# Kernel tuning notes

Measured on AMD Instinct MI355X. Metric: run time of the kernel, lower is better.

Reference implementation:

```python
import jax, jax.numpy as jnp
import numpy as np

DIM = 256
FEATURE_SCALE = 4
NMS_THRESHOLD = 8.0
PRE_NMS_TOPK = 2048
MAX_OUTPUT = 256
MIN_SCORE = 0.2


def conv3d_same(x, w, b):
    # x: [D,H,W,Cin], w: [3,3,3,Cin,Cout] -> [D,H,W,Cout], SAME padding (flax default)
    y = jax.lax.conv_general_dilated(
        x[None], w, window_strides=(1, 1, 1), padding="SAME",
        dimension_numbers=("NDHWC", "DHWIO", "NDHWC"))
    return y[0] + b


def setup_inputs() -> dict:
    key = jax.random.key(0)
    ks = jax.random.split(key, 8)
    D, H, W, C = 16, 64, 64, 256
    feature = jax.random.normal(ks[0], (D, H, W, C), jnp.float32)
    mask = jax.random.bernoulli(ks[1], 0.8, (D * FEATURE_SCALE, H * FEATURE_SCALE, W * FEATURE_SCALE))
    s3a = 1.0 / np.sqrt(27 * C)
    s3b = 1.0 / np.sqrt(27 * DIM)
    s1 = 1.0 / np.sqrt(DIM)
    w0 = jax.random.normal(ks[2], (3, 3, 3, C, DIM), jnp.float32) * s3a
    b0 = jnp.zeros((DIM,), jnp.float32)
    w1 = jax.random.normal(ks[3], (3, 3, 3, DIM, DIM), jnp.float32) * s3b
    b1 = jnp.zeros((DIM,), jnp.float32)
    w_logit = jax.random.normal(ks[4], (DIM, 1), jnp.float32) * s1
    b_logit = jnp.zeros((1,), jnp.float32)
    w_reg = jax.random.normal(ks[5], (DIM, 3), jnp.float32) * s1
    b_reg = jnp.zeros((3,), jnp.float32)
    return dict(feature=feature, mask=mask, w0=w0, b0=b0, w1=w1, b1=b1,
                w_logit=w_logit, b_logit=b_logit, w_reg=w_reg, b_reg=b_reg)


def reference(feature, mask, w0, b0, w1, b1, w_logit, b_logit, w_reg, b_reg):
    # ---- feature mixing: n_layers=2 of conv3d + gelu (flax gelu is approximate/tanh) ----
    x = jax.nn.gelu(conv3d_same(feature, w0, b0))
    x = jax.nn.gelu(conv3d_same(x, w1, b1))
    D, H, W = x.shape[:3]

    # ---- detection block: 1x1 convs are pointwise dense layers ----
    logits = (x @ w_logit + b_logit)[..., 0].reshape(-1)          # [N]
    regressions = (x @ w_reg + b_reg)                              # [D,H,W,3]
    ref_locs = (jnp.moveaxis(jnp.mgrid[:D, :H, :W], 0, -1) + 0.5) * FEATURE_SCALE
    pred_locs = (ref_locs + regressions * FEATURE_SCALE).reshape(-1, 3)  # [N,3]

    # ---- generate_predictions: sigmoid scores, pre-NMS top-k, greedy distance NMS ----
    scores = jax.nn.sigmoid(logits)
    top_scores, idx = jax.lax.top_k(scores, PRE_NMS_TOPK)          # sorted desc
    top_locs = pred_locs[idx]                                      # [K,3]
    d2 = ((top_locs[:, None, :] - top_locs[None, :, :]) ** 2).sum(-1)  # [K,K]
    th2 = NMS_THRESHOLD * NMS_THRESHOLD

    def step(suppressed, i):
        keep_i = (~suppressed[i]) & (top_scores[i] >= MIN_SCORE)
        suppressed = suppressed | (keep_i & (d2[i] < th2))
        return suppressed, keep_i

    _, keep = jax.lax.scan(step, jnp.zeros((PRE_NMS_TOPK,), bool), jnp.arange(PRE_NMS_TOPK))
    sel_scores = jnp.where(keep, top_scores, 0.0)
    out_scores, oidx = jax.lax.top_k(sel_scores, MAX_OUTPUT)       # [M]
    out_locs = top_locs[oidx]                                      # [M,3]

    # ---- mask gather: floor/clip/index, zero out-of-mask scores ----
    pli = jnp.floor(out_locs).astype(jnp.int32)
    bound = jnp.array(mask.shape, jnp.int32) - 1
    plc = jnp.clip(pli, 0, bound)
    in_range = (pli == plc).all(axis=1)
    masked = jnp.where(in_range, mask[plc[:, 0], plc[:, 1], plc[:, 2]], False)
    out_scores = jnp.where(masked, out_scores, 0.0)

    return jnp.concatenate([out_locs, out_scores[:, None]], axis=-1)  # [M,4] = (z,y,x,score)
```

## Files before the change

### kernel.cpp

```cpp
#include <hip/hip_runtime.h>
#include <math.h>

#define Dz 16
#define Hy 64
#define Wx 64
#define CHN 256
#define NVOX (Dz*Hy*Wx)
#define TOPK 2048
#define MAXOUT 256
#define CAND_CAP 4096
#define NBCAP 16

typedef __attribute__((ext_vector_type(8))) _Float16 h8;
typedef __attribute__((ext_vector_type(8))) unsigned short u16x8;
typedef __attribute__((ext_vector_type(4))) float f32x4;

__device__ __forceinline__ float gelu_tanh(float x) {
    return 0.5f*x*(1.0f + tanhf(0.7978845608028654f*(x + 0.044715f*x*x*x)));
}
__device__ __forceinline__ unsigned f2sort(float f) {
    unsigned u = __float_as_uint(f);
    return (u & 0x80000000u) ? ~u : (u | 0x80000000u);
}
__device__ __forceinline__ float sort2f(unsigned s) {
    unsigned u = (s & 0x80000000u) ? (s & 0x7fffffffu) : ~s;
    return __uint_as_float(u);
}

#define MFMA(d, a, b) d = __builtin_amdgcn_mfma_f32_16x16x32_f16(a, b, d, 0, 0, 0)

__global__ __launch_bounds__(256) void pack_w_kernel(const float* __restrict__ w0,
        const float* __restrict__ w1, u16x8* __restrict__ wpk0,
        u16x8* __restrict__ wpk1) {
    int id = blockIdx.x*256 + threadIdx.x;
    int l = (id >= 221184) ? 1 : 0;
    int r = id - l*221184;
    int lane = r & 63, ng = (r >> 6) & 15, kbg = (r >> 10) & 7, t = r >> 13;
    const float* w = l ? w1 : w0;
    u16x8* dst = l ? wpk1 : wpk0;
    h8 hv = {0,0,0,0,0,0,0,0}, lv = {0,0,0,0,0,0,0,0};
    #pragma unroll
    for (int j = 0; j < 8; ++j) {
        int k = kbg*32 + (lane >> 4)*8 + j;
        int co = ng*16 + (lane & 15);
        float v = w[((size_t)t*CHN + k)*CHN + co];
        _Float16 h = (_Float16)v;
        hv[j] = h;
        lv[j] = (_Float16)(v - (float)h);
    }
    size_t base = (((size_t)(t*8 + kbg)*16 + ng)*2)*64 + lane;
    dst[base]      = __builtin_bit_cast(u16x8, hv);
    dst[base + 64] = __builtin_bit_cast(u16x8, lv);
}

template<int LAYER>
__global__ __launch_bounds__(512, 4) void conv_kernel(
        const float* __restrict__ fsrc,
        const unsigned short* __restrict__ hhi, const unsigned short* __restrict__ hlo,
        const u16x8* __restrict__ wpk, const float* __restrict__ bias,
        unsigned short* __restrict__ ohi, unsigned short* __restrict__ olo,
        const float* __restrict__ wlog, const float* __restrict__ blog,
        const float* __restrict__ wreg, const float* __restrict__ breg,
        float* __restrict__ locs, unsigned long long* __restrict__ keys,
        unsigned* __restrict__ hist) {
    __shared__ h8 sm[4224];
    const int tid = threadIdx.x;
    const int lane = tid & 63, w = tid >> 6;
    const int yo = w >> 2, wn = w & 3;
    const int lr = lane & 15, lg = lane >> 4;
    const int z = blockIdx.y, y0 = blockIdx.x*2;

    f32x4 acc[4][4];
    #pragma unroll
    for (int m = 0; m < 4; ++m)
        #pragma unroll
        for (int n = 0; n < 4; ++n) acc[m][n] = (f32x4){0.f,0.f,0.f,0.f};

    for (int dz = 0; dz < 3; ++dz) {
        const int zz = z + dz - 1;
        for (int kc = 0; kc < 4; ++kc) {
            __syncthreads();
            if (LAYER == 0) {
                for (int cidx = tid; cidx < 2112; cidx += 512) {
                    int cd = cidx & 7;
                    int rr = cidx >> 3;
                    int r = rr % 66, iy = rr / 66;
                    int ygl = y0 - 1 + iy, xin = r - 1;
                    h8 hv = {0,0,0,0,0,0,0,0}, lv = {0,0,0,0,0,0,0,0};
                    if (((unsigned)zz < (unsigned)Dz) & ((unsigned)ygl < (unsigned)Hy)
                        & ((unsigned)xin < (unsigned)Wx)) {
                        const float* s = fsrc + ((size_t)((zz*Hy + ygl)*Wx + xin))*CHN
                                              + kc*64 + cd*8;
                        float4 t0 = *(const float4*)s;
                        float4 t1 = *(const float4*)(s + 4);
                        float vv[8] = {t0.x,t0.y,t0.z,t0.w,t1.x,t1.y,t1.z,t1.w};
                        #pragma unroll
                        for (int j = 0; j < 8; ++j) {
                            _Float16 h = (_Float16)vv[j];
                            hv[j] = h;
                            lv[j] = (_Float16)(vv[j] - (float)h);
                        }
                    }
                    int sl = cd ^ (r & 7);
                    sm[(iy*66 + r)*8 + sl] = hv;
                    sm[2112 + (iy*66 + r)*8 + sl] = lv;
                }
            } else {
                for (int cidx = tid; cidx < 4224; cidx += 512) {
                    int c = cidx & 7;
                    int rr = cidx >> 3;
                    int r = rr % 66, tt = rr / 66;
                    int p = tt >> 2, iy = tt & 3;
                    int ygl = y0 - 1 + iy, xin = r - 1;
                    u16x8 v = {0,0,0,0,0,0,0,0};
                    if (((unsigned)zz < (unsigned)Dz) & ((unsigned)ygl < (unsigned)Hy)
                        & ((unsigned)xin < (unsigned)Wx)) {
                        const unsigned short* bp = p ? hlo : hhi;
                        v = *(const u16x8*)(bp + ((size_t)((zz*Hy + ygl)*Wx + xin))*CHN
                                               + kc*64 + (size_t)((c ^ (r & 7)))*8);
                    }
                    sm[cidx] = __builtin_bit_cast(h8, v);
                }
            }
            __syncthreads();
            for (int dy = 0; dy < 3; ++dy) {
                const int iyA = yo + dy;
                const h8* As = sm + iyA*528;
                #pragma unroll
                for (int dx = 0; dx < 3; ++dx) {
                    const int tap = (dz*3 + dy)*3 + dx;
                    #pragma unroll
                    for (int kb = 0; kb < 2; ++kb) {
                        const int kbg = kc*2 + kb;
                        const u16x8* wb = wpk + ((size_t)(tap*8 + kbg)*32 + wn*8)*64 + lane;
                        h8 bh[4];
                        #pragma unroll
                        for (int n = 0; n < 4; ++n)
                            bh[n] = __builtin_bit_cast(h8, wb[(size_t)n*128]);
                        #pragma unroll
                        for (int m = 0; m < 4; ++m) {
                            const int r = m*16 + lr + dx;
                            const int sl = (kb*4 + lg) ^ (r & 7);
                            h8 ah = As[r*8 + sl];
                            h8 al = As[2112 + r*8 + sl];
                            #pragma unroll
                            for (int n = 0; n < 4; ++n) {
                                MFMA(acc[m][n], ah, bh[n]);
                                MFMA(acc[m][n], al, bh[n]);
                            }
                        }
                        h8 bl[4];
                        #pragma unroll
                        for (int n = 0; n < 4; ++n)
                            bl[n] = __builtin_bit_cast(h8, wb[(size_t)n*128 + 64]);
                        #pragma unroll
                        for (int m = 0; m < 4; ++m) {
                            const int r = m*16 + lr + dx;
                            const int sl = (kb*4 + lg) ^ (r & 7);
                            h8 ah = As[r*8 + sl];
                            #pragma unroll
                            for (int n = 0; n < 4; ++n) MFMA(acc[m][n], ah, bl[n]);
                        }
                    }
                }
            }
        }
    }

    float bn[4];
    #pragma unroll
    for (int n = 0; n < 4; ++n) bn[n] = bias[wn*64 + n*16 + lr];

    if (LAYER == 0) {
        const int ygl = y0 + yo;
        #pragma unroll
        for (int m = 0; m < 4; ++m) {
            #pragma unroll
            for (int rg = 0; rg < 4; ++rg) {
                const int x = m*16 + lg*4 + rg;
                const size_t vbase = ((size_t)((z*Hy + ygl)*Wx + x))*CHN;
                #pragma unroll
                for (int n = 0; n < 4; ++n) {
                    const int co = wn*64 + n*16 + lr;
                    float g = gelu_tanh(acc[m][n][rg] + bn[n]);
                    _Float16 h = (_Float16)g;
                    _Float16 l = (_Float16)(g - (float)h);
                    ohi[vbase + co] = __builtin_bit_cast(unsigned short, h);
                    olo[vbase + co] = __builtin_bit_cast(unsigned short, l);
                }
            }
        }
    } else {
        float wl[4], wr0[4], wr1[4], wr2[4];
        #pragma unroll
        for (int n = 0; n < 4; ++n) {
            const int co = wn*64 + n*16 + lr;
            wl[n] = wlog[co];
            wr0[n] = wreg[co*3 + 0]; wr1[n] = wreg[co*3 + 1]; wr2[n] = wreg[co*3 + 2];
        }
        float p[4][16];
        #pragma unroll
        for (int c = 0; c < 4; ++c)
            #pragma unroll
            for (int xi = 0; xi < 16; ++xi) p[c][xi] = 0.f;
        #pragma unroll
        for (int m = 0; m < 4; ++m)
            #pragma unroll
            for (int rg = 0; rg < 4; ++rg) {
                const int xi = m*4 + rg;
                #pragma unroll
                for (int n = 0; n < 4; ++n) {
                    float g = gelu_tanh(acc[m][n][rg] + bn[n]);
                    p[0][xi] += g*wl[n];
                    p[1][xi] += g*wr0[n];
                    p[2][xi] += g*wr1[n];
                    p[3][xi] += g*wr2[n];
                }
            }
        #pragma unroll
        for (int st = 0; st < 4; ++st) {
            const int s = 1 << st;
            #pragma unroll
            for (int c = 0; c < 4; ++c)
                #pragma unroll
                for (int xi = 0; xi < 16; ++xi)
                    p[c][xi] += __shfl_xor(p[c][xi], s, 64);
        }
        __syncthreads();
        float* det = (float*)sm;
        if (lr == 0) {
            #pragma unroll
            for (int m = 0; m < 4; ++m)
                #pragma unroll
                for (int rg = 0; rg < 4; ++rg) {
                    const int x = m*16 + lg*4 + rg;
                    #pragma unroll
                    for (int c = 0; c < 4; ++c)
                        det[((yo*64 + x)*4 + c)*4 + wn] = p[c][m*4 + rg];
                }
        }
        __syncthreads();
        {
            const int yo2 = tid >> 8, x = (tid >> 2) & 63, chn = tid & 3;
            const float* dp = det + ((yo2*64 + x)*4 + chn)*4;
            float s = dp[0] + dp[1] + dp[2] + dp[3];
            const int ygl = y0 + yo2;
            const int vg = (z*Hy + ygl)*Wx + x;
            if (chn == 0) {
                float logit = s + blog[0];
                float score = 1.f/(1.f + expf(-logit));
                unsigned sb = f2sort(score);
                keys[vg] = ((unsigned long long)sb << 32)
                         | (unsigned long long)(0xFFFFFFFFu - (unsigned)vg);
                atomicAdd(&hist[sb >> 12], 1u);
            } else {
                float coord = (chn == 1) ? (float)z : (chn == 2) ? (float)ygl : (float)x;
                float loc = (coord + 0.5f)*4.0f + (s + breg[chn-1])*4.0f;
                locs[(size_t)vg*3 + (chn-1)] = loc;
            }
        }
    }
}

__global__ void zero_kernel(unsigned* __restrict__ hist, unsigned* __restrict__ counter) {
    int i = blockIdx.x*blockDim.x + threadIdx.x;
    if (i < (1 << 20)) hist[i] = 0u;
    if (i == 0) counter[0] = 0u;
}

__global__ __launch_bounds__(1024) void find_cut_kernel(const unsigned* __restrict__ hist,
                                                        unsigned* __restrict__ cutp) {
    __shared__ unsigned long long psum[1024];
    __shared__ unsigned h2[1024];
    __shared__ int sh_cb;
    __shared__ unsigned long long sh_acc;
    int t = threadIdx.x;
    unsigned long long s = 0;
    const unsigned* hp = hist + (size_t)t*1024;
    for (int b = 0; b < 1024; ++b) s += hp[b];
    psum[t] = s;
    __syncthreads();
    if (t == 0) {
        unsigned long long acc = 0; int cb = 0;
        for (int c = 1023; c >= 0; --c) {
            if (acc + psum[c] >= TOPK) { cb = c; break; }
            acc += psum[c];
        }
        sh_cb = cb; sh_acc = acc;
    }
    __syncthreads();
    int cb = sh_cb;
    h2[t] = hist[(size_t)cb*1024 + t];
    __syncthreads();
    if (t == 0) {
        unsigned long long acc = sh_acc; int cut = cb*1024;
        for (int b = 1023; b >= 0; --b) {
            acc += h2[b];
            if (acc >= TOPK) { cut = cb*1024 + b; break; }
        }
        cutp[0] = ((unsigned)cut) << 12;
    }
}

__global__ void compact_kernel(const unsigned long long* __restrict__ keys,
                               const unsigned* __restrict__ cutp,
                               unsigned* __restrict__ counter,
                               unsigned long long* __restrict__ cand) {
    int i = blockIdx.x*blockDim.x + threadIdx.x;
    unsigned thr = cutp[0];
    unsigned long long k = keys[i];
    if ((unsigned)(k >> 32) >= thr) {
        unsigned p = atomicAdd(counter, 1u);
        if (p < CAND_CAP) cand[p] = k;
    }
}

__global__ __launch_bounds__(512) void rank_kernel(const unsigned* __restrict__ counter,
        const unsigned long long* __restrict__ cand, const float* __restrict__ locs,
        float* __restrict__ sscoreG, float* __restrict__ slzG,
        float* __restrict__ slyG, float* __restrict__ slxG) {
    __shared__ unsigned long long kbuf[CAND_CAP];
    int t = threadIdx.x;
    int g = blockIdx.x*512 + t;
    int M = (int)*counter; if (M > CAND_CAP) M = CAND_CAP;
    for (int i = t; i < CAND_CAP; i += 512) kbuf[i] = (i < M) ? cand[i] : 0ull;
    __syncthreads();
    if (g >= M) return;
    unsigned long long mykey = kbuf[g];
    int rank = 0;
    for (int j = 0; j < M; ++j) rank += (kbuf[j] > mykey) ? 1 : 0;
    if (rank < TOPK) {
        unsigned idx = 0xFFFFFFFFu - (unsigned)(mykey & 0xFFFFFFFFull);
        sscoreG[rank] = sort2f((unsigned)(mykey >> 32));
        slzG[rank] = locs[(size_t)idx*3 + 0];
        slyG[rank] = locs[(size_t)idx*3 + 1];
        slxG[rank] = locs[(size_t)idx*3 + 2];
    }
}

__global__ __launch_bounds__(256) void nbr_kernel(const float* __restrict__ slzG,
        const float* __restrict__ slyG, const float* __restrict__ slxG,
        unsigned short* __restrict__ nbidx, unsigned char* __restrict__ nbcnt) {
    __shared__ float bz[TOPK], by[TOPK], bx[TOPK];
    int t = threadIdx.x;
    int g = blockIdx.x*256 + t;
    for (int i = t; i < TOPK; i += 256) { bz[i]=slzG[i]; by[i]=slyG[i]; bx[i]=slxG[i]; }
    __syncthreads();
    float myz = bz[g], myy = by[g], myx = bx[g];
    int cnt = 0;
    for (int j = 0; j < TOPK; ++j) {
        float dz = bz[j]-myz, dy = by[j]-myy, dx = bx[j]-myx;
        float d2 = dz*dz + dy*dy + dx*dx;
        if (d2 < 64.0f && j != g) {
            if (cnt < NBCAP) nbidx[(size_t)g*NBCAP + cnt] = (unsigned short)j;
            cnt++;
        }
    }
    nbcnt[g] = (unsigned char)min(cnt, 255);
}

__global__ __launch_bounds__(512) void nms_kernel(const float* __restrict__ sscoreG,
        const float* __restrict__ slzG, const float* __restrict__ slyG,
        const float* __restrict__ slxG, const unsigned short* __restrict__ nbidx,
        const unsigned char* __restrict__ nbcnt, const int* __restrict__ mask,
        float* __restrict__ out) {
    __shared__ float ssc[TOPK], slz[TOPK], sly[TOPK], slx[TOPK];
    __shared__ unsigned short snb[TOPK*NBCAP];
    __shared__ unsigned char scnt[TOPK];
    __shared__ unsigned char supf[TOPK];
    __shared__ unsigned char keepB[TOPK];
    __shared__ unsigned keepw[64];
    __shared__ int wpre[64];
    __shared__ int sh_nk;
    int t = threadIdx.x;
    for (int i = t; i < TOPK; i += 512) {
        ssc[i] = sscoreG[i]; slz[i] = slzG[i]; sly[i] = slyG[i]; slx[i] = slxG[i];
        scnt[i] = nbcnt[i]; supf[i] = 0; keepB[i] = 0;
    }
    for (int i = t; i < TOPK*NBCAP/8; i += 512)
        ((uint4*)snb)[i] = ((const uint4*)nbidx)[i];
    __syncthreads();
    if (t < 64) {
        const int l = t;
        float cz[32], cy[32], cx[32];
        #pragma unroll
        for (int j = 0; j < 32; ++j) {
            cz[j] = slz[l*32 + j]; cy[j] = sly[l*32 + j]; cx[j] = slx[l*32 + j];
        }
        int keeps = 0;
        for (int i = 0; i < TOPK; ++i) {
            bool kept = (supf[i] == 0) && (ssc[i] >= 0.2f);
            if (kept) {
                if (l == 0) keepB[i] = 1;
                ++keeps;
                const int cnt = scnt[i];
                if (cnt <= NBCAP) {
                    if (l < cnt) supf[snb[i*NBCAP + l]] = 1;
                } else {
                    const float pz = slz[i], py = sly[i], px = slx[i];
                    #pragma unroll
                    for (int j = 0; j < 32; ++j) {
                        float dz = cz[j]-pz, dy = cy[j]-py, dx = cx[j]-px;
                        if (dz*dz + dy*dy + dx*dx < 64.0f) supf[l*32 + j] = 1;
                    }
                }
                asm volatile("s_waitcnt lgkmcnt(0)" ::: "memory");
                if (keeps >= MAXOUT) break;
            }
        }
    }
    __syncthreads();
    if (t < 64) {
        unsigned wmask = 0u;
        for (int j = 0; j < 32; ++j) wmask |= (keepB[t*32 + j] ? 1u : 0u) << j;
        keepw[t] = wmask;
    }
    __syncthreads();
    if (t < 64) {
        int p = 0;
        for (int j = 0; j < t; ++j) p += __popc(keepw[j]);
        wpre[t] = p;
        if (t == 63) sh_nk = p + __popc(keepw[63]);
    }
    __syncthreads();
    const int nk = sh_nk;
    for (int i = t; i < TOPK; i += 512) {
        unsigned w = keepw[i >> 5];
        bool kp = (w >> (i & 31)) & 1u;
        int rk = wpre[i >> 5] + __popc(w & ((1u << (i & 31)) - 1u));
        int slot = kp ? rk : (nk + (i - rk));
        if (slot < MAXOUT) {
            float lz = slz[i], ly = sly[i], lx = slx[i];
            float sc = kp ? ssc[i] : 0.f;
            int iz = (int)floorf(lz), iy = (int)floorf(ly), ix = (int)floorf(lx);
            int cz2 = min(max(iz,0),Dz*4-1), cy2 = min(max(iy,0),Hy*4-1), cx2 = min(max(ix,0),Wx*4-1);
            bool inr = (iz==cz2) && (iy==cy2) && (ix==cx2);
            float osc = (inr && mask[((size_t)cz2*(Hy*4) + cy2)*(Wx*4) + cx2] != 0) ? sc : 0.f;
            out[slot*4+0] = lz; out[slot*4+1] = ly; out[slot*4+2] = lx; out[slot*4+3] = osc;
        }
    }
}

extern "C" void kernel_launch(void* const* d_in, const int* in_sizes, int n_in,
                              void* d_out, int out_size, void* d_ws, size_t ws_size,
                              hipStream_t stream) {
    const float* feature = (const float*)d_in[0];
    const int*   mask    = (const int*)d_in[1];
    const float* w0   = (const float*)d_in[2];
    const float* b0   = (const float*)d_in[3];
    const float* w1   = (const float*)d_in[4];
    const float* b1   = (const float*)d_in[5];
    const float* wlog = (const float*)d_in[6];
    const float* blog = (const float*)d_in[7];
    const float* wreg = (const float*)d_in[8];
    const float* breg = (const float*)d_in[9];

    char* ws = (char*)d_ws;
    size_t off = 0;
    unsigned short* h1hi = (unsigned short*)(ws + off); off += (size_t)NVOX*CHN*2;
    unsigned short* h1lo = (unsigned short*)(ws + off); off += (size_t)NVOX*CHN*2;
    u16x8* wpk0 = (u16x8*)(ws + off);               off += (size_t)442368*16;
    u16x8* wpk1 = (u16x8*)(ws + off);               off += (size_t)442368*16;
    unsigned long long* keys = (unsigned long long*)(ws + off); off += (size_t)NVOX*8;
    float* locs = (float*)(ws + off);               off += (size_t)NVOX*3*4;
    unsigned* hist = (unsigned*)(ws + off);         off += (size_t)(1u<<20)*4;
    unsigned* counter = (unsigned*)(ws + off);      off += 256;
    unsigned* cutp = counter + 1;
    unsigned long long* cand = (unsigned long long*)(ws + off); off += (size_t)CAND_CAP*8;
    float* sscoreG = (float*)(ws + off);            off += (size_t)TOPK*4;
    float* slzG = (float*)(ws + off);               off += (size_t)TOPK*4;
    float* slyG = (float*)(ws + off);               off += (size_t)TOPK*4;
    float* slxG = (float*)(ws + off);               off += (size_t)TOPK*4;
    unsigned short* nbidx = (unsigned short*)(ws + off); off += (size_t)TOPK*NBCAP*2;
    unsigned char* nbcnt = (unsigned char*)(ws + off);   off += (size_t)TOPK;
    if (ws_size < off) return;

    zero_kernel<<<4096, 256, 0, stream>>>(hist, counter);
    pack_w_kernel<<<1728, 256, 0, stream>>>(w0, w1, wpk0, wpk1);
    dim3 cgrid(Hy/2, Dz);
    conv_kernel<0><<<cgrid, 512, 0, stream>>>(feature, nullptr, nullptr, wpk0, b0,
                                              h1hi, h1lo,
                                              nullptr, nullptr, nullptr, nullptr,
                                              nullptr, nullptr, nullptr);
    conv_kernel<1><<<cgrid, 512, 0, stream>>>(nullptr, h1hi, h1lo, wpk1, b1,
                                              nullptr, nullptr,
                                              wlog, blog, wreg, breg,
                                              locs, keys, hist);
    find_cut_kernel<<<1, 1024, 0, stream>>>(hist, cutp);
    compact_kernel<<<NVOX/256, 256, 0, stream>>>(keys, cutp, counter, cand);
    rank_kernel<<<CAND_CAP/512, 512, 0, stream>>>(counter, cand, locs,
                                                  sscoreG, slzG, slyG, slxG);
    nbr_kernel<<<TOPK/256, 256, 0, stream>>>(slzG, slyG, slxG, nbidx, nbcnt);
    nms_kernel<<<1, 512, 0, stream>>>(sscoreG, slzG, slyG, slxG, nbidx, nbcnt,
                                      mask, (float*)d_out);
}
```

Before: 1.489 ms.

## Stage conv tiles via async global-to-LDS loads and shrink top-k histogram

Conv input tiles are now copied straight from global memory into LDS with global_load_lds, using a zero buffer as the source for padded positions. Layer 0 stores raw fp32 in LDS and splits each value into fp16 hi/lo inside the MFMA loop. Separately, the score histogram shrinks from 1M to 64K bins with a parallel prefix-scan cut search, and the zeroing kernel is fused into weight packing. Rank, neighbour and NMS data is packed as float4, and the NMS loop stops at the last candidate above the score threshold. The fp32 staging repeats the hi/lo conversion per tap, adding VALU work that competes with MFMA issue in layer 0.

```diff
diff --git a/kernel.cpp b/kernel.cpp
--- a/kernel.cpp
+++ b/kernel.cpp
@@ -10,6 +10,7 @@
 #define MAXOUT 256
 #define CAND_CAP 4096
 #define NBCAP 16
+#define NHIST 65536
 
 typedef __attribute__((ext_vector_type(8))) _Float16 h8;
 typedef __attribute__((ext_vector_type(8))) unsigned short u16x8;
@@ -29,35 +30,81 @@
 
 #define MFMA(d, a, b) d = __builtin_amdgcn_mfma_f32_16x16x32_f16(a, b, d, 0, 0, 0)
 
-__global__ __launch_bounds__(256) void pack_w_kernel(const float* __restrict__ w0,
+__device__ __forceinline__ void gl_lds16(const void* g, void* l) {
+    __builtin_amdgcn_global_load_lds(
+        (const __attribute__((address_space(1))) void*)g,
+        (__attribute__((address_space(3))) void*)l, 16, 0, 0);
+}
+
+__global__ __launch_bounds__(256) void prep_kernel(const float* __restrict__ w0,
         const float* __restrict__ w1, u16x8* __restrict__ wpk0,
-        u16x8* __restrict__ wpk1) {
-    int id = blockIdx.x*256 + threadIdx.x;
-    int l = (id >= 221184) ? 1 : 0;
-    int r = id - l*221184;
-    int lane = r & 63, ng = (r >> 6) & 15, kbg = (r >> 10) & 7, t = r >> 13;
-    const float* w = l ? w1 : w0;
-    u16x8* dst = l ? wpk1 : wpk0;
-    h8 hv = {0,0,0,0,0,0,0,0}, lv = {0,0,0,0,0,0,0,0};
-    #pragma unroll
-    for (int j = 0; j < 8; ++j) {
-        int k = kbg*32 + (lane >> 4)*8 + j;
-        int co = ng*16 + (lane & 15);
-        float v = w[((size_t)t*CHN + k)*CHN + co];
-        _Float16 h = (_Float16)v;
-        hv[j] = h;
-        lv[j] = (_Float16)(v - (float)h);
-    }
-    size_t base = (((size_t)(t*8 + kbg)*16 + ng)*2)*64 + lane;
-    dst[base]      = __builtin_bit_cast(u16x8, hv);
-    dst[base + 64] = __builtin_bit_cast(u16x8, lv);
+        u16x8* __restrict__ wpk1, unsigned* __restrict__ hist,
+        unsigned* __restrict__ counter, float4* __restrict__ zerob) {
+    int b = blockIdx.x, t = threadIdx.x;
+    if (b < 1728) {
+        int id = b*256 + t;
+        int l = (id >= 221184) ? 1 : 0;
+        int r = id - l*221184;
+        int lane = r & 63, ng = (r >> 6) & 15, kbg = (r >> 10) & 7, tp = r >> 13;
+        const float* w = l ? w1 : w0;
+        u16x8* dst = l ? wpk1 : wpk0;
+        h8 hv, lv;
+        #pragma unroll
+        for (int j = 0; j < 8; ++j) {
+            int k = kbg*32 + (lane >> 4)*8 + j;
+            int co = ng*16 + (lane & 15);
+            float v = w[((size_t)tp*CHN + k)*CHN + co];
+            _Float16 h = (_Float16)v;
+            hv[j] = h;
+            lv[j] = (_Float16)(v - (float)h);
+        }
+        size_t base = (((size_t)(tp*8 + kbg)*16 + ng)*2)*64 + lane;
+        dst[base]      = __builtin_bit_cast(u16x8, hv);
+        dst[base + 64] = __builtin_bit_cast(u16x8, lv);
+    } else {
+        int zb = b - 1728;
+        int i = zb*256 + t;
+        hist[i] = 0u; hist[i + 16384] = 0u; hist[i + 32768] = 0u; hist[i + 49152] = 0u;
+        if (zb == 0 && t == 0) counter[0] = 0u;
+        if (zb == 0 && t == 2) *zerob = make_float4(0.f, 0.f, 0.f, 0.f);
+    }
+}
+
+template<int LAYER>
+__device__ __forceinline__ void stage_chunk(int cidx, void* ldst,
+        const float* f32in, const unsigned short* hhi, const unsigned short* hlo,
+        const float4* zerob, int zz, bool zok, int y0, int kc) {
+    const void* src;
+    if (LAYER == 0) {
+        int c = cidx & 15, rr = cidx >> 4;
+        int r = rr % 66, iy = rr / 66;
+        int ygl = y0 - 1 + iy, xin = r - 1;
+        bool ok = zok & ((unsigned)ygl < (unsigned)Hy) & ((unsigned)xin < (unsigned)Wx);
+        int cs = c ^ ((r & 7) << 1);
+        src = ok ? (const void*)(f32in + ((size_t)(((size_t)zz*Hy + ygl)*Wx + xin))*CHN
+                                 + kc*64 + cs*4)
+                 : (const void*)zerob;
+    } else {
+        int c = cidx & 7, rr = cidx >> 3;
+        int r = rr % 66, tt = rr / 66;
+        int p = tt >> 2, iy = tt & 3;
+        int ygl = y0 - 1 + iy, xin = r - 1;
+        bool ok = zok & ((unsigned)ygl < (unsigned)Hy) & ((unsigned)xin < (unsigned)Wx);
+        int cs = c ^ (r & 7);
+        const unsigned short* bp = p ? hlo : hhi;
+        src = ok ? (const void*)(bp + ((size_t)(((size_t)zz*Hy + ygl)*Wx + xin))*CHN
+                                 + kc*64 + cs*8)
+                 : (const void*)zerob;
+    }
+    gl_lds16(src, ldst);
 }
 
 template<int LAYER>
 __global__ __launch_bounds__(512, 4) void conv_kernel(
-        const float* __restrict__ fsrc,
+        const float* __restrict__ f32in,
         const unsigned short* __restrict__ hhi, const unsigned short* __restrict__ hlo,
         const u16x8* __restrict__ wpk, const float* __restrict__ bias,
+        const float4* __restrict__ zerob,
         unsigned short* __restrict__ ohi, unsigned short* __restrict__ olo,
         const float* __restrict__ wlog, const float* __restrict__ blog,
         const float* __restrict__ wreg, const float* __restrict__ breg,
@@ -69,6 +116,7 @@
     const int yo = w >> 2, wn = w & 3;
     const int lr = lane & 15, lg = lane >> 4;
     const int z = blockIdx.y, y0 = blockIdx.x*2;
+    const int wbs = tid & ~63;
 
     f32x4 acc[4][4];
     #pragma unroll
@@ -78,54 +126,20 @@
 
     for (int dz = 0; dz < 3; ++dz) {
         const int zz = z + dz - 1;
+        const bool zok = (unsigned)zz < (unsigned)Dz;
         for (int kc = 0; kc < 4; ++kc) {
             __syncthreads();
-            if (LAYER == 0) {
-                for (int cidx = tid; cidx < 2112; cidx += 512) {
-                    int cd = cidx & 7;
-                    int rr = cidx >> 3;
-                    int r = rr % 66, iy = rr / 66;
-                    int ygl = y0 - 1 + iy, xin = r - 1;
-                    h8 hv = {0,0,0,0,0,0,0,0}, lv = {0,0,0,0,0,0,0,0};
-                    if (((unsigned)zz < (unsigned)Dz) & ((unsigned)ygl < (unsigned)Hy)
-                        & ((unsigned)xin < (unsigned)Wx)) {
-                        const float* s = fsrc + ((size_t)((zz*Hy + ygl)*Wx + xin))*CHN
-                                              + kc*64 + cd*8;
-                        float4 t0 = *(const float4*)s;
-                        float4 t1 = *(const float4*)(s + 4);
-                        float vv[8] = {t0.x,t0.y,t0.z,t0.w,t1.x,t1.y,t1.z,t1.w};
-                        #pragma unroll
-                        for (int j = 0; j < 8; ++j) {
-                            _Float16 h = (_Float16)vv[j];
-                            hv[j] = h;
-                            lv[j] = (_Float16)(vv[j] - (float)h);
-                        }
-                    }
-                    int sl = cd ^ (r & 7);
-                    sm[(iy*66 + r)*8 + sl] = hv;
-                    sm[2112 + (iy*66 + r)*8 + sl] = lv;
-                }
-            } else {
-                for (int cidx = tid; cidx < 4224; cidx += 512) {
-                    int c = cidx & 7;
-                    int rr = cidx >> 3;
-                    int r = rr % 66, tt = rr / 66;
-                    int p = tt >> 2, iy = tt & 3;
-                    int ygl = y0 - 1 + iy, xin = r - 1;
-                    u16x8 v = {0,0,0,0,0,0,0,0};
-                    if (((unsigned)zz < (unsigned)Dz) & ((unsigned)ygl < (unsigned)Hy)
-                        & ((unsigned)xin < (unsigned)Wx)) {
-                        const unsigned short* bp = p ? hlo : hhi;
-                        v = *(const u16x8*)(bp + ((size_t)((zz*Hy + ygl)*Wx + xin))*CHN
-                                               + kc*64 + (size_t)((c ^ (r & 7)))*8);
-                    }
-                    sm[cidx] = __builtin_bit_cast(h8, v);
-                }
-            }
+            #pragma unroll
+            for (int k = 0; k < 8; ++k)
+                stage_chunk<LAYER>(k*512 + tid, (void*)&sm[k*512 + wbs],
+                                   f32in, hhi, hlo, zerob, zz, zok, y0, kc);
+            if (tid < 128)
+                stage_chunk<LAYER>(4096 + tid, (void*)&sm[4096 + wbs],
+                                   f32in, hhi, hlo, zerob, zz, zok, y0, kc);
+            asm volatile("s_waitcnt vmcnt(0)" ::: "memory");
             __syncthreads();
             for (int dy = 0; dy < 3; ++dy) {
                 const int iyA = yo + dy;
-                const h8* As = sm + iyA*528;
                 #pragma unroll
                 for (int dx = 0; dx < 3; ++dx) {
                     const int tap = (dz*3 + dy)*3 + dx;
@@ -140,9 +154,23 @@
                         #pragma unroll
                         for (int m = 0; m < 4; ++m) {
                             const int r = m*16 + lr + dx;
-                            const int sl = (kb*4 + lg) ^ (r & 7);
-                            h8 ah = As[r*8 + sl];
-                            h8 al = As[2112 + r*8 + sl];
+                            h8 ah, al;
+                            if (LAYER == 0) {
+                                const f32x4* Af = (const f32x4*)sm + ((size_t)iyA*66 + r)*16;
+                                int s0 = (kb*8 + lg*2) ^ ((r & 7) << 1);
+                                f32x4 a0 = Af[s0], a1 = Af[s0 | 1];
+                                #pragma unroll
+                                for (int j = 0; j < 4; ++j) {
+                                    _Float16 h0 = (_Float16)a0[j];
+                                    ah[j] = h0; al[j] = (_Float16)(a0[j] - (float)h0);
+                                    _Float16 h1 = (_Float16)a1[j];
+                                    ah[4+j] = h1; al[4+j] = (_Float16)(a1[j] - (float)h1);
+                                }
+                            } else {
+                                const int sl = (kb*4 + lg) ^ (r & 7);
+                                ah = sm[((size_t)iyA*66 + r)*8 + sl];
+                                al = sm[2112 + ((size_t)iyA*66 + r)*8 + sl];
+                            }
                             #pragma unroll
                             for (int n = 0; n < 4; ++n) {
                                 MFMA(acc[m][n], ah, bh[n]);
@@ -156,8 +184,20 @@
                         #pragma unroll
                         for (int m = 0; m < 4; ++m) {
                             const int r = m*16 + lr + dx;
-                            const int sl = (kb*4 + lg) ^ (r & 7);
-                            h8 ah = As[r*8 + sl];
+                            h8 ah;
+                            if (LAYER == 0) {
+                                const f32x4* Af = (const f32x4*)sm + ((size_t)iyA*66 + r)*16;
+                                int s0 = (kb*8 + lg*2) ^ ((r & 7) << 1);
+                                f32x4 a0 = Af[s0], a1 = Af[s0 | 1];
+                                #pragma unroll
+                                for (int j = 0; j < 4; ++j) {
+                                    ah[j] = (_Float16)a0[j];
+                                    ah[4+j] = (_Float16)a1[j];
+                                }
+                            } else {
+                                const int sl = (kb*4 + lg) ^ (r & 7);
+                                ah = sm[((size_t)iyA*66 + r)*8 + sl];
+                            }
                             #pragma unroll
                             for (int n = 0; n < 4; ++n) MFMA(acc[m][n], ah, bl[n]);
                         }
@@ -252,7 +292,7 @@
                 unsigned sb = f2sort(score);
                 keys[vg] = ((unsigned long long)sb << 32)
                          | (unsigned long long)(0xFFFFFFFFu - (unsigned)vg);
-                atomicAdd(&hist[sb >> 12], 1u);
+                atomicAdd(&hist[sb >> 16], 1u);
             } else {
                 float coord = (chn == 1) ? (float)z : (chn == 2) ? (float)ygl : (float)x;
                 float loc = (coord + 0.5f)*4.0f + (s + breg[chn-1])*4.0f;
@@ -262,43 +302,38 @@
     }
 }
 
-__global__ void zero_kernel(unsigned* __restrict__ hist, unsigned* __restrict__ counter) {
-    int i = blockIdx.x*blockDim.x + threadIdx.x;
-    if (i < (1 << 20)) hist[i] = 0u;
-    if (i == 0) counter[0] = 0u;
-}
-
 __global__ __launch_bounds__(1024) void find_cut_kernel(const unsigned* __restrict__ hist,
                                                         unsigned* __restrict__ cutp) {
-    __shared__ unsigned long long psum[1024];
-    __shared__ unsigned h2[1024];
+    __shared__ unsigned ps[1024];
+    __shared__ unsigned fs[64];
     __shared__ int sh_cb;
-    __shared__ unsigned long long sh_acc;
+    __shared__ unsigned sh_acc;
     int t = threadIdx.x;
-    unsigned long long s = 0;
-    const unsigned* hp = hist + (size_t)t*1024;
-    for (int b = 0; b < 1024; ++b) s += hp[b];
-    psum[t] = s;
-    __syncthreads();
-    if (t == 0) {
-        unsigned long long acc = 0; int cb = 0;
-        for (int c = 1023; c >= 0; --c) {
-            if (acc + psum[c] >= TOPK) { cb = c; break; }
-            acc += psum[c];
-        }
-        sh_cb = cb; sh_acc = acc;
-    }
-    __syncthreads();
-    int cb = sh_cb;
-    h2[t] = hist[(size_t)cb*1024 + t];
-    __syncthreads();
-    if (t == 0) {
-        unsigned long long acc = sh_acc; int cut = cb*1024;
-        for (int b = 1023; b >= 0; --b) {
-            acc += h2[b];
-            if (acc >= TOPK) { cut = cb*1024 + b; break; }
-        }
-        cutp[0] = ((unsigned)cut) << 12;
+    unsigned s = 0;
+    const unsigned* hp = hist + (size_t)t*64;
+    for (int j = 0; j < 64; ++j) s += hp[j];
+    ps[t] = s;
+    __syncthreads();
+    for (int off = 1; off < 1024; off <<= 1) {
+        unsigned v = ps[t] + ((t + off < 1024) ? ps[t + off] : 0u);
+        __syncthreads();
+        ps[t] = v;
+        __syncthreads();
+    }
+    if (ps[t] >= TOPK && (t == 1023 || ps[t+1] < TOPK)) {
+        sh_cb = t; sh_acc = (t == 1023) ? 0u : ps[t+1];
+    }
+    __syncthreads();
+    int cb = sh_cb; unsigned acc = sh_acc;
+    if (t < 64) {
+        unsigned f = acc;
+        for (int u = t; u < 64; ++u) f += hist[(size_t)cb*64 + u];
+        fs[t] = f;
+    }
+    __syncthreads();
+    if (t < 64) {
+        if (fs[t] >= TOPK && (t == 63 || fs[t+1] < TOPK))
+            cutp[0] = ((unsigned)(cb*64 + t)) << 16;
     }
 }
 
@@ -315,15 +350,14 @@
     }
 }
 
-__global__ __launch_bounds__(512) void rank_kernel(const unsigned* __restrict__ counter,
+__global__ __launch_bounds__(128) void rank_kernel(const unsigned* __restrict__ counter,
         const unsigned long long* __restrict__ cand, const float* __restrict__ locs,
-        float* __restrict__ sscoreG, float* __restrict__ slzG,
-        float* __restrict__ slyG, float* __restrict__ slxG) {
+        float4* __restrict__ loc4G) {
     __shared__ unsigned long long kbuf[CAND_CAP];
     int t = threadIdx.x;
-    int g = blockIdx.x*512 + t;
+    int g = blockIdx.x*128 + t;
     int M = (int)*counter; if (M > CAND_CAP) M = CAND_CAP;
-    for (int i = t; i < CAND_CAP; i += 512) kbuf[i] = (i < M) ? cand[i] : 0ull;
+    for (int i = t; i < CAND_CAP; i += 128) kbuf[i] = (i < M) ? cand[i] : 0ull;
     __syncthreads();
     if (g >= M) return;
     unsigned long long mykey = kbuf[g];
@@ -331,25 +365,27 @@
     for (int j = 0; j < M; ++j) rank += (kbuf[j] > mykey) ? 1 : 0;
     if (rank < TOPK) {
         unsigned idx = 0xFFFFFFFFu - (unsigned)(mykey & 0xFFFFFFFFull);
-        sscoreG[rank] = sort2f((unsigned)(mykey >> 32));
-        slzG[rank] = locs[(size_t)idx*3 + 0];
-        slyG[rank] = locs[(size_t)idx*3 + 1];
-        slxG[rank] = locs[(size_t)idx*3 + 2];
-    }
-}
-
-__global__ __launch_bounds__(256) void nbr_kernel(const float* __restrict__ slzG,
-        const float* __restrict__ slyG, const float* __restrict__ slxG,
+        float4 v;
+        v.x = locs[(size_t)idx*3 + 0];
+        v.y = locs[(size_t)idx*3 + 1];
+        v.z = locs[(size_t)idx*3 + 2];
+        v.w = sort2f((unsigned)(mykey >> 32));
+        loc4G[rank] = v;
+    }
+}
+
+__global__ __launch_bounds__(64) void nbr_kernel(const float4* __restrict__ loc4G,
         unsigned short* __restrict__ nbidx, unsigned char* __restrict__ nbcnt) {
-    __shared__ float bz[TOPK], by[TOPK], bx[TOPK];
+    __shared__ float4 b4[TOPK];
     int t = threadIdx.x;
-    int g = blockIdx.x*256 + t;
-    for (int i = t; i < TOPK; i += 256) { bz[i]=slzG[i]; by[i]=slyG[i]; bx[i]=slxG[i]; }
-    __syncthreads();
-    float myz = bz[g], myy = by[g], myx = bx[g];
+    int g = blockIdx.x*64 + t;
+    for (int i = t; i < TOPK; i += 64) b4[i] = loc4G[i];
+    __syncthreads();
+    float4 me = b4[g];
     int cnt = 0;
     for (int j = 0; j < TOPK; ++j) {
-        float dz = bz[j]-myz, dy = by[j]-myy, dx = bx[j]-myx;
+        float4 o = b4[j];
+        float dz = o.x - me.x, dy = o.y - me.y, dx = o.z - me.z;
         float d2 = dz*dz + dy*dy + dx*dx;
         if (d2 < 64.0f && j != g) {
             if (cnt < NBCAP) nbidx[(size_t)g*NBCAP + cnt] = (unsigned short)j;
@@ -359,12 +395,10 @@
     nbcnt[g] = (unsigned char)min(cnt, 255);
 }
 
-__global__ __launch_bounds__(512) void nms_kernel(const float* __restrict__ sscoreG,
-        const float* __restrict__ slzG, const float* __restrict__ slyG,
-        const float* __restrict__ slxG, const unsigned short* __restrict__ nbidx,
-        const unsigned char* __restrict__ nbcnt, const int* __restrict__ mask,
-        float* __restrict__ out) {
-    __shared__ float ssc[TOPK], slz[TOPK], sly[TOPK], slx[TOPK];
+__global__ __launch_bounds__(512) void nms_kernel(const float4* __restrict__ loc4G,
+        const unsigned short* __restrict__ nbidx, const unsigned char* __restrict__ nbcnt,
+        const int* __restrict__ mask, float* __restrict__ out) {
+    __shared__ float4 p4[TOPK];
     __shared__ unsigned short snb[TOPK*NBCAP];
     __shared__ unsigned char scnt[TOPK];
     __shared__ unsigned char supf[TOPK];
@@ -374,8 +408,7 @@
     __shared__ int sh_nk;
     int t = threadIdx.x;
     for (int i = t; i < TOPK; i += 512) {
-        ssc[i] = sscoreG[i]; slz[i] = slzG[i]; sly[i] = slyG[i]; slx[i] = slxG[i];
-        scnt[i] = nbcnt[i]; supf[i] = 0; keepB[i] = 0;
+        p4[i] = loc4G[i]; scnt[i] = nbcnt[i]; supf[i] = 0; keepB[i] = 0;
     }
     for (int i = t; i < TOPK*NBCAP/8; i += 512)
         ((uint4*)snb)[i] = ((const uint4*)nbidx)[i];
@@ -385,11 +418,18 @@
         float cz[32], cy[32], cx[32];
         #pragma unroll
         for (int j = 0; j < 32; ++j) {
-            cz[j] = slz[l*32 + j]; cy[j] = sly[l*32 + j]; cx[j] = slx[l*32 + j];
-        }
+            float4 v = p4[l*32 + j];
+            cz[j] = v.x; cy[j] = v.y; cx[j] = v.z;
+        }
+        int myok = 0;
+        #pragma unroll
+        for (int j = 0; j < 32; ++j) myok += (p4[l*32 + j].w >= 0.2f) ? 1 : 0;
+        #pragma unroll
+        for (int s = 1; s < 64; s <<= 1) myok += __shfl_xor(myok, s, 64);
+        const int NS = myok;
         int keeps = 0;
-        for (int i = 0; i < TOPK; ++i) {
-            bool kept = (supf[i] == 0) && (ssc[i] >= 0.2f);
+        for (int i = 0; i < NS; ++i) {
+            bool kept = (supf[i] == 0);
             if (kept) {
                 if (l == 0) keepB[i] = 1;
                 ++keeps;
@@ -397,10 +437,10 @@
                 if (cnt <= NBCAP) {
                     if (l < cnt) supf[snb[i*NBCAP + l]] = 1;
                 } else {
-                    const float pz = slz[i], py = sly[i], px = slx[i];
+                    float4 pv = p4[i];
                     #pragma unroll
                     for (int j = 0; j < 32; ++j) {
-                        float dz = cz[j]-pz, dy = cy[j]-py, dx = cx[j]-px;
+                        float dz = cz[j]-pv.x, dy = cy[j]-pv.y, dx = cx[j]-pv.z;
                         if (dz*dz + dy*dy + dx*dx < 64.0f) supf[l*32 + j] = 1;
                     }
                 }
@@ -430,8 +470,9 @@
         int rk = wpre[i >> 5] + __popc(w & ((1u << (i & 31)) - 1u));
         int slot = kp ? rk : (nk + (i - rk));
         if (slot < MAXOUT) {
-            float lz = slz[i], ly = sly[i], lx = slx[i];
-            float sc = kp ? ssc[i] : 0.f;
+            float4 v = p4[i];
+            float lz = v.x, ly = v.y, lx = v.z;
+            float sc = kp ? v.w : 0.f;
             int iz = (int)floorf(lz), iy = (int)floorf(ly), ix = (int)floorf(lx);
             int cz2 = min(max(iz,0),Dz*4-1), cy2 = min(max(iy,0),Hy*4-1), cx2 = min(max(ix,0),Wx*4-1);
             bool inr = (iz==cz2) && (iy==cy2) && (ix==cx2);
@@ -463,34 +504,29 @@
     u16x8* wpk1 = (u16x8*)(ws + off);               off += (size_t)442368*16;
     unsigned long long* keys = (unsigned long long*)(ws + off); off += (size_t)NVOX*8;
     float* locs = (float*)(ws + off);               off += (size_t)NVOX*3*4;
-    unsigned* hist = (unsigned*)(ws + off);         off += (size_t)(1u<<20)*4;
+    unsigned* hist = (unsigned*)(ws + off);         off += (size_t)NHIST*4;
     unsigned* counter = (unsigned*)(ws + off);      off += 256;
     unsigned* cutp = counter + 1;
+    float4* zerob = (float4*)(ws + off);            off += 256;
     unsigned long long* cand = (unsigned long long*)(ws + off); off += (size_t)CAND_CAP*8;
-    float* sscoreG = (float*)(ws + off);            off += (size_t)TOPK*4;
-    float* slzG = (float*)(ws + off);               off += (size_t)TOPK*4;
-    float* slyG = (float*)(ws + off);               off += (size_t)TOPK*4;
-    float* slxG = (float*)(ws + off);               off += (size_t)TOPK*4;
+    float4* loc4G = (float4*)(ws + off);            off += (size_t)TOPK*16;
     unsigned short* nbidx = (unsigned short*)(ws + off); off += (size_t)TOPK*NBCAP*2;
     unsigned char* nbcnt = (unsigned char*)(ws + off);   off += (size_t)TOPK;
     if (ws_size < off) return;
 
-    zero_kernel<<<4096, 256, 0, stream>>>(hist, counter);
-    pack_w_kernel<<<1728, 256, 0, stream>>>(w0, w1, wpk0, wpk1);
+    prep_kernel<<<1792, 256, 0, stream>>>(w0, w1, wpk0, wpk1, hist, counter, zerob);
     dim3 cgrid(Hy/2, Dz);
     conv_kernel<0><<<cgrid, 512, 0, stream>>>(feature, nullptr, nullptr, wpk0, b0,
-                                              h1hi, h1lo,
+                                              zerob, h1hi, h1lo,
                                               nullptr, nullptr, nullptr, nullptr,
                                               nullptr, nullptr, nullptr);
     conv_kernel<1><<<cgrid, 512, 0, stream>>>(nullptr, h1hi, h1lo, wpk1, b1,
-                                              nullptr, nullptr,
+                                              zerob, nullptr, nullptr,
                                               wlog, blog, wreg, breg,
                                               locs, keys, hist);
     find_cut_kernel<<<1, 1024, 0, stream>>>(hist, cutp);
     compact_kernel<<<NVOX/256, 256, 0, stream>>>(keys, cutp, counter, cand);
-    rank_kernel<<<CAND_CAP/512, 512, 0, stream>>>(counter, cand, locs,
-                                                  sscoreG, slzG, slyG, slxG);
-    nbr_kernel<<<TOPK/256, 256, 0, stream>>>(slzG, slyG, slxG, nbidx, nbcnt);
-    nms_kernel<<<1, 512, 0, stream>>>(sscoreG, slzG, slyG, slxG, nbidx, nbcnt,
-                                      mask, (float*)d_out);
-}
+    rank_kernel<<<CAND_CAP/128, 128, 0, stream>>>(counter, cand, locs, loc4G);
+    nbr_kernel<<<TOPK/64, 64, 0, stream>>>(loc4G, nbidx, nbcnt);
+    nms_kernel<<<1, 512, 0, stream>>>(loc4G, nbidx, nbcnt, mask, (float*)d_out);
+}
```

Result: slower. 1.560 ms (+4.8%).
